# Performance work log

Measured on AMD Instinct MI355X. Metric: run time of the kernel, lower is better.

The kernel has to match this reference:

```python
import jax, jax.numpy as jnp
import numpy as np

NUM_CHANNELS = 64  # d per group
T_ITERS = 5
EPS = 1e-05


def setup_inputs() -> dict:
    key = jax.random.key(0)
    kx, = jax.random.split(key, 1)
    X = jax.random.normal(kx, (64, 256, 56, 56), dtype=jnp.float32)
    weight = jnp.ones((1, 256, 1, 1), dtype=jnp.float32)
    bias = jnp.zeros((1, 256, 1, 1), dtype=jnp.float32)
    return {"X": X, "weight": weight, "bias": bias}


def reference(X, weight, bias):
    B, C, H, W = X.shape
    nc = NUM_CHANNELS
    g = C // nc
    # (C, B, H, W) -> (g, nc, m) with m = B*H*W
    x = jnp.transpose(X, (1, 0, 2, 3)).reshape(g, nc, -1)
    m = x.shape[-1]
    mean = x.mean(-1, keepdims=True)                      # (g, nc, 1)
    xc = x - mean
    I = jnp.broadcast_to(jnp.eye(nc, dtype=X.dtype), (g, nc, nc))
    # Sigma = eps*I + (1/m) * xc @ xc^T
    Sigma = EPS * I + jnp.einsum('gdm,gem->gde', xc, xc) / m
    # rTr = 1 / trace(Sigma) per group
    rTr = (1.0 / jnp.einsum('gii->g', Sigma))[:, None, None]  # (g,1,1)
    Sigma_N = Sigma * rTr
    # Newton-Schulz iteration: P <- 1.5*P - 0.5*P^3 @ Sigma_N
    P = I
    for _ in range(T_ITERS):
        P3 = jnp.einsum('gij,gjk,gkl->gil', P, P, P)
        P = 1.5 * P - 0.5 * jnp.einsum('gij,gjk->gik', P3, Sigma_N)
    wm = P * jnp.sqrt(rTr)                                 # whitening matrix (g, nc, nc)
    xn = jnp.einsum('gde,gem->gdm', wm, xc)                # whitened data
    X_hat = jnp.transpose(xn.reshape(C, B, H, W), (1, 0, 2, 3))
    return X_hat * weight + bias
```

## Files before the change

### kernel.cpp

```cpp
#include <hip/hip_runtime.h>
#include <hip/hip_bf16.h>
#include <math.h>


#define EPS_F 1e-5f

using f32x4v = __attribute__((ext_vector_type(4))) float;
using f32x2v = __attribute__((ext_vector_type(2))) float;
using short8 = __attribute__((ext_vector_type(8))) short;
using u32x4  = __attribute__((ext_vector_type(4))) unsigned int;
using u32x2  = __attribute__((ext_vector_type(2))) unsigned int;

constexpr int Cc  = 256;
constexpr int HWc = 3136;
constexpr int CHW = Cc * HWc;
constexpr float Mf = 200704.0f;
constexpr int GX  = 196;
constexpr int LDB = 72;

constexpr int WS_SUM  = 0;
constexpr int WS_G    = 256;
constexpr int WS_WM   = WS_G + 16384;
constexpr int WS_BETA = WS_WM + 16384;
constexpr int WS_SLAB = WS_BETA + 256;
constexpr int WS_SSUM = WS_SLAB + 784 * 4096;

__device__ __forceinline__ unsigned cvtpk(float lo, float hi) {
    __hip_bfloat162 h = __float22bfloat162_rn(float2{lo, hi});
    unsigned u;
    __builtin_memcpy(&u, &h, 4);
    return u;
}

__device__ __forceinline__ unsigned short bf16rn(float v) {
    unsigned u = __builtin_bit_cast(unsigned, v);
    u += 0x7FFFu + ((u >> 16) & 1u);
    return (unsigned short)(u >> 16);
}
__device__ __forceinline__ float frombf(unsigned short h) {
    unsigned u = (unsigned)h << 16;
    return __builtin_bit_cast(float, u);
}

__device__ __forceinline__ f32x4v mfma16(short8 a, short8 b, f32x4v c) {
    return __builtin_amdgcn_mfma_f32_16x16x32_bf16(a, b, c, 0, 0, 0);
}

extern "C" __global__ __launch_bounds__(256, 4)
void k_gram(const float* __restrict__ X, float* __restrict__ ws) {
    __shared__ __align__(16) unsigned short tg[2][2][64 * LDB];
    const int g = blockIdx.y, bx = blockIdx.x, tid = threadIdx.x;
    const int lane = tid & 63, w = tid >> 6;
    const int row = tid >> 2, mo = (tid & 3) << 4;
    const int l15 = lane & 15, lg = lane >> 4;
    const int CBi0 = (w >> 1) << 1, CBj0 = (w & 1) << 1;
    const float* Xg = X + (size_t)g * 64 * HWc;

    f32x4v acc[2][2];
    #pragma unroll
    for (int i = 0; i < 2; ++i)
        #pragma unroll
        for (int j = 0; j < 2; ++j) acc[i][j] = (f32x4v){0.f, 0.f, 0.f, 0.f};
    float csum = 0.0f;

    f32x4v curA[4], curB[4];
    auto loadt = [&](int t, f32x4v* cur) {
        const int b = t / 49, hw0 = (t - b * 49) << 6;
        const float* p = Xg + (size_t)b * CHW + (size_t)row * HWc + hw0 + mo;
        cur[0] = *(const f32x4v*)(p);      cur[1] = *(const f32x4v*)(p + 4);
        cur[2] = *(const f32x4v*)(p + 8);  cur[3] = *(const f32x4v*)(p + 12);
    };
    auto packt = [&](const f32x4v* cur, unsigned short* dstbuf) {
        unsigned pk[8];
        #pragma unroll
        for (int i = 0; i < 4; ++i) {
            csum += (cur[i].x + cur[i].y) + (cur[i].z + cur[i].w);
            pk[2*i]   = cvtpk(cur[i].x, cur[i].y);
            pk[2*i+1] = cvtpk(cur[i].z, cur[i].w);
        }
        unsigned short* dst = dstbuf + row * LDB + mo;
        *(u32x4*)(dst)     = (u32x4){pk[0], pk[1], pk[2], pk[3]};
        *(u32x4*)(dst + 8) = (u32x4){pk[4], pk[5], pk[6], pk[7]};
    };
    auto comp = [&](const unsigned short* T) {
        #pragma unroll
        for (int s = 0; s < 2; ++s) {
            const int ko = 8 * lg + 32 * s;
            const short8 a0 = *(const short8*)&T[(CBi0 * 16      + l15) * LDB + ko];
            const short8 a1 = *(const short8*)&T[((CBi0+1) * 16  + l15) * LDB + ko];
            const short8 b0 = *(const short8*)&T[(CBj0 * 16      + l15) * LDB + ko];
            const short8 b1 = *(const short8*)&T[((CBj0+1) * 16  + l15) * LDB + ko];
            acc[0][0] = mfma16(a0, b0, acc[0][0]);
            acc[0][1] = mfma16(a0, b1, acc[0][1]);
            acc[1][0] = mfma16(a1, b0, acc[1][0]);
            acc[1][1] = mfma16(a1, b1, acc[1][1]);
        }
    };

    loadt(bx, curA);
    loadt(bx + GX, curB);

    int buf = 0;
    for (int kk = 0; kk < 8; ++kk) {
        packt(curA, tg[buf][0]);
        packt(curB, tg[buf][1]);
        __syncthreads();
        if (kk < 7) {
            loadt(bx + GX * (2*kk + 2), curA);
            loadt(bx + GX * (2*kk + 3), curB);
        }
        comp(tg[buf][0]);
        comp(tg[buf][1]);
        buf ^= 1;
    }

    csum += __shfl_down(csum, 1, 4);
    csum += __shfl_down(csum, 2, 4);
    if ((tid & 3) == 0)
        ws[WS_SSUM + (g * GX + bx) * 64 + row] = csum;

    float* Gp = ws + WS_SLAB + (size_t)(g * GX + bx) * 4096;
    #pragma unroll
    for (int ci = 0; ci < 2; ++ci)
        #pragma unroll
        for (int cj = 0; cj < 2; ++cj)
            #pragma unroll
            for (int reg = 0; reg < 4; ++reg) {
                const int r = (CBi0 + ci) * 16 + lg * 4 + reg;
                const int c = (CBj0 + cj) * 16 + l15;
                Gp[r * 64 + c] = acc[ci][cj][reg];
            }
}

extern "C" __global__ __launch_bounds__(256)
void k_reduce(float* __restrict__ ws) {
    __shared__ float part[4][64];
    const int g = blockIdx.y, chunk = blockIdx.x, tid = threadIdx.x;
    const int c63 = tid & 63, q = tid >> 6;
    const float* p = ws + WS_SLAB + (size_t)g * GX * 4096
                   + (size_t)(q * 49) * 4096 + chunk * 64 + c63;
    float s = 0.f;
    #pragma unroll 7
    for (int i = 0; i < 49; ++i) { s += *p; p += 4096; }
    part[q][c63] = s;
    __syncthreads();
    if (tid < 64)
        ws[WS_G + g * 4096 + chunk * 64 + tid] =
            (part[0][tid] + part[1][tid]) + (part[2][tid] + part[3][tid]);

    if (chunk == 0 && tid < 64) {
        const float* qq = ws + WS_SSUM + (size_t)g * GX * 64 + tid;
        float a0 = 0.f, a1 = 0.f, a2 = 0.f, a3 = 0.f;
        #pragma unroll 7
        for (int s4 = 0; s4 < 49; ++s4) {
            a0 += qq[0];
            a1 += qq[64];
            a2 += qq[128];
            a3 += qq[192];
            qq += 256;
        }
        ws[WS_SUM + g * 64 + tid] = (a0 + a1) + (a2 + a3);
    }
}

extern "C" __global__ __launch_bounds__(512)
void k_solve(const float* __restrict__ weight, const float* __restrict__ bias,
             float* __restrict__ ws) {
    __shared__ __align__(16) unsigned short PMh[128 * LDB], PMl[128 * LDB];
    __shared__ __align__(16) unsigned short Wh[64 * LDB], Wl[64 * LDB];
    __shared__ float mean_s[64], diag_s[64];
    __shared__ float red;

    const int g = blockIdx.x, tid = threadIdx.x;
    const int lane = tid & 63, w = tid >> 6;
    const int l15 = lane & 15, lg = lane >> 4;
    const int r = tid >> 3, ch = (tid & 7) << 3;

    if (tid < 64) mean_s[tid] = ws[WS_SUM + g * 64 + tid] * (1.0f / Mf);
    __syncthreads();

    const float* Gp = ws + WS_G + g * 4096;
    const float mr = mean_s[r];
    float sv[8];
    #pragma unroll
    for (int j = 0; j < 8; ++j) {
        const int c = ch + j;
        float v = Gp[r * 64 + c] * (1.0f / Mf) - mr * mean_s[c];
        if (c == r) { v += EPS_F; diag_s[r] = v; }
        sv[j] = v;
    }
    __syncthreads();
    if (tid == 0) {
        float tr = 0.f;
        #pragma unroll
        for (int i = 0; i < 64; ++i) tr += diag_s[i];
        red = 1.0f / tr;
    }
    __syncthreads();
    const float rtr = red;

    #pragma unroll
    for (int j = 0; j < 8; ++j) {
        const int c = ch + j;
        PMh[r * LDB + c] = (c == r) ? (unsigned short)0x3F80 : (unsigned short)0;
        PMl[r * LDB + c] = 0;
        const float v = sv[j] * rtr;
        const unsigned short h = bf16rn(v);
        PMh[(64 + r) * LDB + c] = h;
        PMl[(64 + r) * LDB + c] = bf16rn(v - frombf(h));
    }
    __syncthreads();

    for (int t = 0; t < 5; ++t) {
        #pragma unroll
        for (int j = 0; j < 8; ++j) {
            const int c = ch + j;
            const float m = frombf(PMh[(64 + r) * LDB + c])
                          + frombf(PMl[(64 + r) * LDB + c]);
            const float wv = ((c == r) ? 1.5f : 0.0f) - 0.5f * m;
            const unsigned short h = bf16rn(wv);
            Wh[r * LDB + c] = h;
            Wl[r * LDB + c] = bf16rn(wv - frombf(h));
        }
        __syncthreads();

        {
            short8 ah[2], al[2];
            #pragma unroll
            for (int s = 0; s < 2; ++s) {
                const int off = (16 * w + l15) * LDB + 8 * lg + 32 * s;
                ah[s] = *(const short8*)&PMh[off];
                al[s] = *(const short8*)&PMl[off];
            }
            f32x4v acc[4];
            #pragma unroll
            for (int cb = 0; cb < 4; ++cb) acc[cb] = (f32x4v){0.f,0.f,0.f,0.f};
            #pragma unroll
            for (int s = 0; s < 2; ++s)
                #pragma unroll
                for (int cb = 0; cb < 4; ++cb) {
                    const int off = (cb * 16 + l15) * LDB + 8 * lg + 32 * s;
                    const short8 bh = *(const short8*)&Wh[off];
                    const short8 bl = *(const short8*)&Wl[off];
                    acc[cb] = mfma16(ah[s], bh, acc[cb]);
                    acc[cb] = mfma16(al[s], bh, acc[cb]);
                    acc[cb] = mfma16(ah[s], bl, acc[cb]);
                }
            #pragma unroll
            for (int cb = 0; cb < 4; ++cb)
                #pragma unroll
                for (int reg = 0; reg < 4; ++reg) {
                    const int row = 16 * w + lg * 4 + reg;
                    const int col = cb * 16 + l15;
                    const float c = acc[cb][reg];
                    const unsigned short h = bf16rn(c);
                    PMh[row * LDB + col] = h;
                    PMl[row * LDB + col] = bf16rn(c - frombf(h));
                }
        }
        __syncthreads();

        if (t < 4) {
            const int rb = 4 + (w >> 1);
            const int cb0 = (w & 1) << 1;
            short8 ah[2], al[2];
            #pragma unroll
            for (int s = 0; s < 2; ++s) {
                const int off = (rb * 16 + l15) * LDB + 8 * lg + 32 * s;
                ah[s] = *(const short8*)&PMh[off];
                al[s] = *(const short8*)&PMl[off];
            }
            __syncthreads();
            f32x4v acc[2];
            #pragma unroll
            for (int c2 = 0; c2 < 2; ++c2) acc[c2] = (f32x4v){0.f,0.f,0.f,0.f};
            #pragma unroll
            for (int s = 0; s < 2; ++s)
                #pragma unroll
                for (int c2 = 0; c2 < 2; ++c2) {
                    const int off = ((cb0 + c2) * 16 + l15) * LDB + 8 * lg + 32 * s;
                    const short8 bh = *(const short8*)&Wh[off];
                    const short8 bl = *(const short8*)&Wl[off];
                    acc[c2] = mfma16(ah[s], bh, acc[c2]);
                    acc[c2] = mfma16(al[s], bh, acc[c2]);
                    acc[c2] = mfma16(ah[s], bl, acc[c2]);
                }
            #pragma unroll
            for (int c2 = 0; c2 < 2; ++c2)
                #pragma unroll
                for (int reg = 0; reg < 4; ++reg) {
                    const int row = rb * 16 + lg * 4 + reg;
                    const int col = (cb0 + c2) * 16 + l15;
                    const float c = acc[c2][reg];
                    const unsigned short h = bf16rn(c);
                    PMh[row * LDB + col] = h;
                    PMl[row * LDB + col] = bf16rn(c - frombf(h));
                }
            __syncthreads();
        }
    }

    const float srtr = sqrtf(rtr);
    const float wr = weight[g * 64 + r];
    float* Wp = ws + WS_WM + g * 4096;
    float part = 0.0f;
    #pragma unroll
    for (int j = 0; j < 8; ++j) {
        const int c = ch + j;
        const float p = frombf(PMh[r * LDB + c]) + frombf(PMl[r * LDB + c]);
        const float wm = p * srtr;
        Wp[r * 64 + c] = wm * wr;
        part += wm * mean_s[c];
    }
    part += __shfl_down(part, 1, 8);
    part += __shfl_down(part, 2, 8);
    part += __shfl_down(part, 4, 8);
    if ((tid & 7) == 0)
        ws[WS_BETA + g * 64 + r] = bias[g * 64 + r] - wr * part;
}

extern "C" __global__ __launch_bounds__(256, 4)
void k_apply(const float* __restrict__ X, const float* __restrict__ ws,
             float* __restrict__ out) {
    __shared__ __align__(16) unsigned short tx[2][2][64 * LDB];
    __shared__ __align__(16) float beta_sh[64];

    const int g = blockIdx.y, bx = blockIdx.x, tid = threadIdx.x;
    const int lane = tid & 63, w = tid >> 6;
    const int l15 = lane & 15, lg = lane >> 4;
    const float* Xg = X + (size_t)g * 64 * HWc;

    {
        unsigned short* wm_s = &tx[0][0][0];
        const float* Wp = ws + WS_WM + g * 4096;
        const int r = tid >> 2, chh = (tid & 3) << 4;
        const float* p = Wp + r * 64 + chh;
        const f32x4v v0 = *(const f32x4v*)(p);      const f32x4v v1 = *(const f32x4v*)(p + 4);
        const f32x4v v2 = *(const f32x4v*)(p + 8);  const f32x4v v3 = *(const f32x4v*)(p + 12);
        unsigned short* dst = &wm_s[r * LDB + chh];
        *(u32x4*)(dst)     = (u32x4){cvtpk(v0.x,v0.y), cvtpk(v0.z,v0.w),
                                     cvtpk(v1.x,v1.y), cvtpk(v1.z,v1.w)};
        *(u32x4*)(dst + 8) = (u32x4){cvtpk(v2.x,v2.y), cvtpk(v2.z,v2.w),
                                     cvtpk(v3.x,v3.y), cvtpk(v3.z,v3.w)};
        if (tid < 64) beta_sh[tid] = ws[WS_BETA + g * 64 + tid];
    }
    __syncthreads();

    const int CB0 = (w >> 1) << 1, MB0 = (w & 1) << 1;
    short8 afrag[2][2];
    {
        const unsigned short* wm_s = &tx[0][0][0];
        #pragma unroll
        for (int ci = 0; ci < 2; ++ci)
            #pragma unroll
            for (int s = 0; s < 2; ++s)
                afrag[ci][s] = *(const short8*)&wm_s[((CB0 + ci) * 16 + l15) * LDB + 8 * lg + 32 * s];
    }

    float betav[2][4]; int crow[2][4];
    #pragma unroll
    for (int ci = 0; ci < 2; ++ci)
        #pragma unroll
        for (int reg = 0; reg < 4; ++reg) {
            const int cl = (CB0 + ci) * 16 + lg * 4 + reg;
            betav[ci][reg] = beta_sh[cl];
            crow[ci][reg]  = (g * 64 + cl) * HWc;
        }
    __syncthreads();

    const int qq = lane >> 4, ss = lane & 15;
    const int ecol = 16 * w + 4 * qq;
    int eoff[4], woff[4];
    #pragma unroll
    for (int jj = 0; jj < 4; ++jj) eoff[jj] = (ecol + jj) * HWc + 4 * ss;
    #pragma unroll
    for (int i = 0; i < 4; ++i) {
        const int m = 4 * ss + i;
        const int rT = 32 * (m >> 5) + 16 * (m & 1) + ((m & 31) >> 1);
        woff[i] = rT * LDB + ecol;
    }
    const int mcb = 32 * (w & 1) + 2 * l15;

    f32x4v curA[4], curB[4];
    auto loadt = [&](int t, f32x4v* cur) {
        const int b = t / 49, hw0 = (t - b * 49) << 6;
        const float* p = Xg + (size_t)b * CHW + hw0;
        #pragma unroll
        for (int jj = 0; jj < 4; ++jj)
            cur[jj] = *(const f32x4v*)(p + eoff[jj]);
    };
    auto packt = [&](const f32x4v* cur, unsigned short* dstbuf) {
        #pragma unroll
        for (int i = 0; i < 4; ++i) {
            const u32x2 d = {cvtpk(cur[0][i], cur[1][i]),
                             cvtpk(cur[2][i], cur[3][i])};
            *(u32x2*)&dstbuf[woff[i]] = d;
        }
    };
    auto compst = [&](const unsigned short* T, int t) {
        f32x4v acc[2][2];
        #pragma unroll
        for (int i = 0; i < 2; ++i)
            #pragma unroll
            for (int j = 0; j < 2; ++j) acc[i][j] = (f32x4v){0.f,0.f,0.f,0.f};
        #pragma unroll
        for (int s = 0; s < 2; ++s) {
            const int ko = 8 * lg + 32 * s;
            const short8 b0 = *(const short8*)&T[(MB0 * 16     + l15) * LDB + ko];
            const short8 b1 = *(const short8*)&T[((MB0+1) * 16 + l15) * LDB + ko];
            acc[0][0] = mfma16(afrag[0][s], b0, acc[0][0]);
            acc[0][1] = mfma16(afrag[0][s], b1, acc[0][1]);
            acc[1][0] = mfma16(afrag[1][s], b0, acc[1][0]);
            acc[1][1] = mfma16(afrag[1][s], b1, acc[1][1]);
        }
        const int b = t / 49, hw0 = (t - b * 49) << 6;
        float* ob = out + (size_t)b * CHW + hw0 + mcb;
        #pragma unroll
        for (int ci = 0; ci < 2; ++ci)
            #pragma unroll
            for (int reg = 0; reg < 4; ++reg) {
                const float bt = betav[ci][reg];
                const f32x2v v = {acc[ci][0][reg] + bt, acc[ci][1][reg] + bt};
                __builtin_nontemporal_store(v, (f32x2v*)(ob + crow[ci][reg]));
            }
    };

    loadt(bx, curA);
    loadt(bx + GX, curB);

    int buf = 0;
    for (int kk = 0; kk < 8; ++kk) {
        packt(curA, tx[buf][0]);
        packt(curB, tx[buf][1]);
        __syncthreads();
        if (kk < 7) {
            loadt(bx + GX * (2*kk + 2), curA);
            loadt(bx + GX * (2*kk + 3), curB);
        }
        compst(tx[buf][0], bx + GX * (2*kk));
        compst(tx[buf][1], bx + GX * (2*kk + 1));
        buf ^= 1;
    }
}

extern "C" void kernel_launch(void* const* d_in, const int* in_sizes, int n_in,
                              void* d_out, int out_size, void* d_ws, size_t ws_size,
                              hipStream_t stream) {
    const float* X      = (const float*)d_in[0];
    const float* weight = (const float*)d_in[1];
    const float* bias   = (const float*)d_in[2];
    float* out = (float*)d_out;
    float* ws  = (float*)d_ws;

    hipLaunchKernelGGL(k_gram,   dim3(GX, 4), dim3(256), 0, stream, X, ws);
    hipLaunchKernelGGL(k_reduce, dim3(64, 4), dim3(256), 0, stream, ws);
    hipLaunchKernelGGL(k_solve,  dim3(4),     dim3(512), 0, stream, weight, bias, ws);
    hipLaunchKernelGGL(k_apply,  dim3(GX, 4), dim3(256), 0, stream, X, ws, out);
}
```

Measured before the change: 134.2 us.

## Fold Newton-Schulz affine into MFMA accumulators; widen apply stores to 16-byte

```diff
diff --git a/kernel.cpp b/kernel.cpp
--- a/kernel.cpp
+++ b/kernel.cpp
@@ -166,15 +166,15 @@
 extern "C" __global__ __launch_bounds__(512)
 void k_solve(const float* __restrict__ weight, const float* __restrict__ bias,
              float* __restrict__ ws) {
-    __shared__ __align__(16) unsigned short PMh[128 * LDB], PMl[128 * LDB];
-    __shared__ __align__(16) unsigned short Wh[64 * LDB], Wl[64 * LDB];
+    __shared__ __align__(16) unsigned short PNh[128 * LDB], PNl[128 * LDB];
+    __shared__ __align__(16) unsigned short Th[64 * LDB], Tl[64 * LDB];
     __shared__ float mean_s[64], diag_s[64];
     __shared__ float red;
 
     const int g = blockIdx.x, tid = threadIdx.x;
     const int lane = tid & 63, w = tid >> 6;
     const int l15 = lane & 15, lg = lane >> 4;
-    const int r = tid >> 3, ch = (tid & 7) << 3;
+    const int r = tid >> 3, ch8 = (tid & 7) << 3;
 
     if (tid < 64) mean_s[tid] = ws[WS_SUM + g * 64 + tid] * (1.0f / Mf);
     __syncthreads();
@@ -184,7 +184,7 @@
     float sv[8];
     #pragma unroll
     for (int j = 0; j < 8; ++j) {
-        const int c = ch + j;
+        const int c = ch8 + j;
         float v = Gp[r * 64 + c] * (1.0f / Mf) - mr * mean_s[c];
         if (c == r) { v += EPS_F; diag_s[r] = v; }
         sv[j] = v;
@@ -201,47 +201,42 @@
 
     #pragma unroll
     for (int j = 0; j < 8; ++j) {
-        const int c = ch + j;
-        PMh[r * LDB + c] = (c == r) ? (unsigned short)0x3F80 : (unsigned short)0;
-        PMl[r * LDB + c] = 0;
-        const float v = sv[j] * rtr;
+        const int c = ch8 + j;
+        PNh[r * LDB + c] = (c == r) ? (unsigned short)0x3F80 : (unsigned short)0;
+        PNl[r * LDB + c] = 0;
+        const float v = sv[j] * rtr * (-0.5f);
         const unsigned short h = bf16rn(v);
-        PMh[(64 + r) * LDB + c] = h;
-        PMl[(64 + r) * LDB + c] = bf16rn(v - frombf(h));
+        PNh[(64 + r) * LDB + c] = h;
+        PNl[(64 + r) * LDB + c] = bf16rn(v - frombf(h));
     }
     __syncthreads();
 
     for (int t = 0; t < 5; ++t) {
-        #pragma unroll
-        for (int j = 0; j < 8; ++j) {
-            const int c = ch + j;
-            const float m = frombf(PMh[(64 + r) * LDB + c])
-                          + frombf(PMl[(64 + r) * LDB + c]);
-            const float wv = ((c == r) ? 1.5f : 0.0f) - 0.5f * m;
-            const unsigned short h = bf16rn(wv);
-            Wh[r * LDB + c] = h;
-            Wl[r * LDB + c] = bf16rn(wv - frombf(h));
-        }
-        __syncthreads();
-
         {
             short8 ah[2], al[2];
             #pragma unroll
             for (int s = 0; s < 2; ++s) {
                 const int off = (16 * w + l15) * LDB + 8 * lg + 32 * s;
-                ah[s] = *(const short8*)&PMh[off];
-                al[s] = *(const short8*)&PMl[off];
+                ah[s] = *(const short8*)&PNh[off];
+                al[s] = *(const short8*)&PNl[off];
             }
             f32x4v acc[4];
             #pragma unroll
-            for (int cb = 0; cb < 4; ++cb) acc[cb] = (f32x4v){0.f,0.f,0.f,0.f};
+            for (int cb = 0; cb < 4; ++cb)
+                #pragma unroll
+                for (int reg = 0; reg < 4; ++reg) {
+                    const int row = 16 * w + 4 * lg + reg;
+                    const int col = cb * 16 + l15;
+                    acc[cb][reg] = 1.5f * (frombf(PNh[row * LDB + col])
+                                         + frombf(PNl[row * LDB + col]));
+                }
             #pragma unroll
             for (int s = 0; s < 2; ++s)
                 #pragma unroll
                 for (int cb = 0; cb < 4; ++cb) {
-                    const int off = (cb * 16 + l15) * LDB + 8 * lg + 32 * s;
-                    const short8 bh = *(const short8*)&Wh[off];
-                    const short8 bl = *(const short8*)&Wl[off];
+                    const int off = (64 + cb * 16 + l15) * LDB + 8 * lg + 32 * s;
+                    const short8 bh = *(const short8*)&PNh[off];
+                    const short8 bl = *(const short8*)&PNl[off];
                     acc[cb] = mfma16(ah[s], bh, acc[cb]);
                     acc[cb] = mfma16(al[s], bh, acc[cb]);
                     acc[cb] = mfma16(ah[s], bl, acc[cb]);
@@ -250,51 +245,69 @@
             for (int cb = 0; cb < 4; ++cb)
                 #pragma unroll
                 for (int reg = 0; reg < 4; ++reg) {
-                    const int row = 16 * w + lg * 4 + reg;
+                    const int row = 16 * w + 4 * lg + reg;
                     const int col = cb * 16 + l15;
                     const float c = acc[cb][reg];
                     const unsigned short h = bf16rn(c);
-                    PMh[row * LDB + col] = h;
-                    PMl[row * LDB + col] = bf16rn(c - frombf(h));
+                    if (w < 4) {
+                        PNh[row * LDB + col] = h;
+                        PNl[row * LDB + col] = bf16rn(c - frombf(h));
+                    } else {
+                        Th[(row - 64) * LDB + col] = h;
+                        Tl[(row - 64) * LDB + col] = bf16rn(c - frombf(h));
+                    }
                 }
         }
         __syncthreads();
 
         if (t < 4) {
-            const int rb = 4 + (w >> 1);
+            const int rb = w >> 1;
             const int cb0 = (w & 1) << 1;
-            short8 ah[2], al[2];
+            short8 tah[2], tal[2];
             #pragma unroll
             for (int s = 0; s < 2; ++s) {
                 const int off = (rb * 16 + l15) * LDB + 8 * lg + 32 * s;
-                ah[s] = *(const short8*)&PMh[off];
-                al[s] = *(const short8*)&PMl[off];
+                tah[s] = *(const short8*)&Th[off];
+                tal[s] = *(const short8*)&Tl[off];
             }
+            short8 bh[2][2], bl[2][2];
+            #pragma unroll
+            for (int c2 = 0; c2 < 2; ++c2)
+                #pragma unroll
+                for (int s = 0; s < 2; ++s) {
+                    const int off = (64 + (cb0 + c2) * 16 + l15) * LDB + 8 * lg + 32 * s;
+                    bh[c2][s] = *(const short8*)&PNh[off];
+                    bl[c2][s] = *(const short8*)&PNl[off];
+                }
+            f32x4v acc[2];
+            #pragma unroll
+            for (int c2 = 0; c2 < 2; ++c2)
+                #pragma unroll
+                for (int reg = 0; reg < 4; ++reg) {
+                    const int row = rb * 16 + 4 * lg + reg;
+                    const int col = (cb0 + c2) * 16 + l15;
+                    acc[c2][reg] = 1.5f * (frombf(Th[row * LDB + col])
+                                         + frombf(Tl[row * LDB + col]));
+                }
             __syncthreads();
-            f32x4v acc[2];
-            #pragma unroll
-            for (int c2 = 0; c2 < 2; ++c2) acc[c2] = (f32x4v){0.f,0.f,0.f,0.f};
             #pragma unroll
             for (int s = 0; s < 2; ++s)
                 #pragma unroll
                 for (int c2 = 0; c2 < 2; ++c2) {
-                    const int off = ((cb0 + c2) * 16 + l15) * LDB + 8 * lg + 32 * s;
-                    const short8 bh = *(const short8*)&Wh[off];
-                    const short8 bl = *(const short8*)&Wl[off];
-                    acc[c2] = mfma16(ah[s], bh, acc[c2]);
-                    acc[c2] = mfma16(al[s], bh, acc[c2]);
-                    acc[c2] = mfma16(ah[s], bl, acc[c2]);
+                    acc[c2] = mfma16(tah[s], bh[c2][s], acc[c2]);
+                    acc[c2] = mfma16(tal[s], bh[c2][s], acc[c2]);
+                    acc[c2] = mfma16(tah[s], bl[c2][s], acc[c2]);
                 }
             #pragma unroll
             for (int c2 = 0; c2 < 2; ++c2)
                 #pragma unroll
                 for (int reg = 0; reg < 4; ++reg) {
-                    const int row = rb * 16 + lg * 4 + reg;
+                    const int row = 64 + rb * 16 + 4 * lg + reg;
                     const int col = (cb0 + c2) * 16 + l15;
                     const float c = acc[c2][reg];
                     const unsigned short h = bf16rn(c);
-                    PMh[row * LDB + col] = h;
-                    PMl[row * LDB + col] = bf16rn(c - frombf(h));
+                    PNh[row * LDB + col] = h;
+                    PNl[row * LDB + col] = bf16rn(c - frombf(h));
                 }
             __syncthreads();
         }
@@ -306,8 +319,8 @@
     float part = 0.0f;
     #pragma unroll
     for (int j = 0; j < 8; ++j) {
-        const int c = ch + j;
-        const float p = frombf(PMh[r * LDB + c]) + frombf(PMl[r * LDB + c]);
+        const int c = ch8 + j;
+        const float p = frombf(PNh[r * LDB + c]) + frombf(PNl[r * LDB + c]);
         const float wm = p * srtr;
         Wp[r * 64 + c] = wm * wr;
         part += wm * mean_s[c];
@@ -346,26 +359,20 @@
     }
     __syncthreads();
 
-    const int CB0 = (w >> 1) << 1, MB0 = (w & 1) << 1;
-    short8 afrag[2][2];
+    short8 afrag[2];
     {
         const unsigned short* wm_s = &tx[0][0][0];
         #pragma unroll
-        for (int ci = 0; ci < 2; ++ci)
-            #pragma unroll
-            for (int s = 0; s < 2; ++s)
-                afrag[ci][s] = *(const short8*)&wm_s[((CB0 + ci) * 16 + l15) * LDB + 8 * lg + 32 * s];
-    }
-
-    float betav[2][4]; int crow[2][4];
-    #pragma unroll
-    for (int ci = 0; ci < 2; ++ci)
-        #pragma unroll
-        for (int reg = 0; reg < 4; ++reg) {
-            const int cl = (CB0 + ci) * 16 + lg * 4 + reg;
-            betav[ci][reg] = beta_sh[cl];
-            crow[ci][reg]  = (g * 64 + cl) * HWc;
-        }
+        for (int s = 0; s < 2; ++s)
+            afrag[s] = *(const short8*)&wm_s[(16 * w + l15) * LDB + 8 * lg + 32 * s];
+    }
+    float betav[4]; int crow[4];
+    #pragma unroll
+    for (int reg = 0; reg < 4; ++reg) {
+        const int cl = 16 * w + lg * 4 + reg;
+        betav[reg] = beta_sh[cl];
+        crow[reg]  = (g * 64 + cl) * HWc;
+    }
     __syncthreads();
 
     const int qq = lane >> 4, ss = lane & 15;
@@ -374,12 +381,7 @@
     #pragma unroll
     for (int jj = 0; jj < 4; ++jj) eoff[jj] = (ecol + jj) * HWc + 4 * ss;
     #pragma unroll
-    for (int i = 0; i < 4; ++i) {
-        const int m = 4 * ss + i;
-        const int rT = 32 * (m >> 5) + 16 * (m & 1) + ((m & 31) >> 1);
-        woff[i] = rT * LDB + ecol;
-    }
-    const int mcb = 32 * (w & 1) + 2 * l15;
+    for (int i = 0; i < 4; ++i) woff[i] = (i * 16 + ss) * LDB + ecol;
 
     f32x4v curA[4], curB[4];
     auto loadt = [&](int t, f32x4v* cur) {
@@ -398,31 +400,27 @@
         }
     };
     auto compst = [&](const unsigned short* T, int t) {
-        f32x4v acc[2][2];
-        #pragma unroll
-        for (int i = 0; i < 2; ++i)
-            #pragma unroll
-            for (int j = 0; j < 2; ++j) acc[i][j] = (f32x4v){0.f,0.f,0.f,0.f};
+        f32x4v acc[4];
+        #pragma unroll
+        for (int mb = 0; mb < 4; ++mb) acc[mb] = (f32x4v){0.f,0.f,0.f,0.f};
         #pragma unroll
         for (int s = 0; s < 2; ++s) {
             const int ko = 8 * lg + 32 * s;
-            const short8 b0 = *(const short8*)&T[(MB0 * 16     + l15) * LDB + ko];
-            const short8 b1 = *(const short8*)&T[((MB0+1) * 16 + l15) * LDB + ko];
-            acc[0][0] = mfma16(afrag[0][s], b0, acc[0][0]);
-            acc[0][1] = mfma16(afrag[0][s], b1, acc[0][1]);
-            acc[1][0] = mfma16(afrag[1][s], b0, acc[1][0]);
-            acc[1][1] = mfma16(afrag[1][s], b1, acc[1][1]);
+            #pragma unroll
+            for (int mb = 0; mb < 4; ++mb) {
+                const short8 b = *(const short8*)&T[(mb * 16 + l15) * LDB + ko];
+                acc[mb] = mfma16(afrag[s], b, acc[mb]);
+            }
         }
         const int b = t / 49, hw0 = (t - b * 49) << 6;
-        float* ob = out + (size_t)b * CHW + hw0 + mcb;
-        #pragma unroll
-        for (int ci = 0; ci < 2; ++ci)
-            #pragma unroll
-            for (int reg = 0; reg < 4; ++reg) {
-                const float bt = betav[ci][reg];
-                const f32x2v v = {acc[ci][0][reg] + bt, acc[ci][1][reg] + bt};
-                __builtin_nontemporal_store(v, (f32x2v*)(ob + crow[ci][reg]));
-            }
+        float* ob = out + (size_t)b * CHW + hw0 + 4 * l15;
+        #pragma unroll
+        for (int reg = 0; reg < 4; ++reg) {
+            const float bt = betav[reg];
+            const f32x4v v = {acc[0][reg] + bt, acc[1][reg] + bt,
+                              acc[2][reg] + bt, acc[3][reg] + bt};
+            __builtin_nontemporal_store(v, (f32x4v*)(ob + crow[reg]));
+        }
     };
 
     loadt(bx, curA);
```

Result: no change. 132.1 us (-1.6%).
